# Kernel optimization log

Hardware: AMD Instinct MI355X
Metric: run time of the kernel (lower is better)

Reference implementation:

```python
import jax, jax.numpy as jnp
import numpy as np

B, L, D = 4, 2048, 512
H, DK = 8, 64          # n_heads, d_k = d_model // n_heads
DF = 2048              # d_ff
W = 9                  # window_size (odd so padding w//2 keeps L windows)


def setup_inputs() -> dict:
    key = jax.random.key(0)
    ks = jax.random.split(key, 12)
    s = 0.02
    p = lambda k, shp: (jax.random.normal(k, shp, jnp.float32) * s)
    return {
        "x": jax.random.normal(ks[0], (B, L, D), jnp.float32),
        "Wq": p(ks[1], (D, D)), "bq": jnp.zeros((D,), jnp.float32),
        "Wk": p(ks[2], (D, D)), "bk": jnp.zeros((D,), jnp.float32),
        "Wv": p(ks[3], (D, D)), "bv": jnp.zeros((D,), jnp.float32),
        "Wo": p(ks[4], (D, D)), "bo": jnp.zeros((D,), jnp.float32),
        "W1": p(ks[5], (D, DF)), "b1": jnp.zeros((DF,), jnp.float32),
        "W2": p(ks[6], (DF, D)), "b2": jnp.zeros((D,), jnp.float32),
        "g1": jnp.ones((D,), jnp.float32), "be1": jnp.zeros((D,), jnp.float32),
        "g2": jnp.ones((D,), jnp.float32), "be2": jnp.zeros((D,), jnp.float32),
    }


def _layer_norm(x, g, b, eps=1e-5):
    m = jnp.mean(x, axis=-1, keepdims=True)
    v = jnp.var(x, axis=-1, keepdims=True)
    return (x - m) * jax.lax.rsqrt(v + eps) * g + b


def reference(x, Wq, bq, Wk, bk, Wv, bv, Wo, bo, W1, b1, W2, b2, g1, be1, g2, be2):
    b, l, d = x.shape
    pad = W // 2
    padded = jnp.pad(x, ((0, 0), (pad, pad), (0, 0)))          # (B, L+W-1, D)
    idx = jnp.arange(l)[:, None] + jnp.arange(W)[None, :]       # (L, W)
    win = padded[:, idx]                                        # (B, L, W, D)

    # per-window full attention (Informer FullAttention, mask_flag=False)
    q = (win @ Wq + bq).reshape(b, l, W, H, DK)
    k = (win @ Wk + bk).reshape(b, l, W, H, DK)
    v = (win @ Wv + bv).reshape(b, l, W, H, DK)
    scale = 1.0 / jnp.sqrt(jnp.float32(DK))
    scores = jnp.einsum('blqhe,blkhe->blhqk', q, k) * scale     # (B, L, H, W, W)
    attn = jax.nn.softmax(scores, axis=-1)
    o = jnp.einsum('blhqk,blkhd->blqhd', attn, v).reshape(b, l, W, d)
    o = o @ Wo + bo                                             # (B, L, W, D)
    new_x = jnp.mean(o, axis=2)                                 # mean-pool over window

    x1 = _layer_norm(x + new_x, g1, be1)

    # pointwise conv FFN (kernel_size=1 Conv1d == Linear), exact GELU
    h = jax.nn.gelu(x1 @ W1 + b1, approximate=False)
    y = h @ W2 + b2
    return _layer_norm(x1 + y, g2, be2)
```

## Files before the change

kernel.cpp:

```cpp
#include <hip/hip_runtime.h>


typedef unsigned short u16;
typedef __attribute__((ext_vector_type(8))) short short8;
typedef __attribute__((ext_vector_type(4))) float floatx4;

#define DEV static __device__ __forceinline__

DEV float b2f(u16 u) {
  union { unsigned int i; float f; } x; x.i = ((unsigned int)u) << 16; return x.f;
}
DEV u16 f2b(float f) {
  union { float f; unsigned int i; } x; x.f = f;
  unsigned int u = x.i + 0x7fffu + ((x.i >> 16) & 1u);
  return (u16)(u >> 16);
}

#define AS1 __attribute__((address_space(1)))
#define AS3 __attribute__((address_space(3)))
DEV void gload_lds16(const void* g, void* l) {
  __builtin_amdgcn_global_load_lds((const AS1 void*)g, (AS3 void*)l, 16, 0, 0);
}

__global__ __launch_bounds__(256) void prep_all(
    const float* __restrict__ Wq, const float* __restrict__ Wk,
    const float* __restrict__ Wo, const float* __restrict__ W1,
    const float* __restrict__ W2, const float* __restrict__ Wv,
    const float* __restrict__ bq, const float* __restrict__ bk,
    const float* __restrict__ bv, const float* __restrict__ x,
    u16* __restrict__ WqkvT, u16* __restrict__ WoT,
    u16* __restrict__ W1T, u16* __restrict__ W2T, u16* __restrict__ Wvb,
    float* __restrict__ bqkv, u16* __restrict__ xb) {
  const int bid = blockIdx.x;
  if (bid >= 3080) {
    const int i = (bid - 3080) * 256 + threadIdx.x;
    float4 v = ((const float4*)x)[i];
    ushort4 o;
    o.x = f2b(v.x); o.y = f2b(v.y); o.z = f2b(v.z); o.w = f2b(v.w);
    ((ushort4*)xb)[i] = o;
    return;
  }
  if (bid >= 3072) {
    const int i = (bid - 3072) * 256 + threadIdx.x;
    if (i < 512) bqkv[i] = bq[i];
    else if (i < 1024) bqkv[i] = bk[i - 512];
    else if (i < 1536) {
      const int c = i - 1024;
      float s = 0.f;
      for (int j = 0; j < 512; ++j) s += bv[j] * Wo[(size_t)j * 512 + c];
      bqkv[i] = s;
    } else bqkv[i] = 0.f;
    return;
  }
  if (bid >= 2816) {
    const int i = (bid - 2816) * 256 + threadIdx.x;
    float4 v = ((const float4*)Wv)[i];
    ushort4 o;
    o.x = f2b(v.x); o.y = f2b(v.y); o.z = f2b(v.z); o.w = f2b(v.w);
    ((ushort4*)Wvb)[i] = o;
    return;
  }
  const float* in; u16* out; int R, C, t;
  if (bid < 256)       { in = Wq; out = WqkvT;          R = 512;  C = 512;  t = bid; }
  else if (bid < 512)  { in = Wk; out = WqkvT + 262144; R = 512;  C = 512;  t = bid - 256; }
  else if (bid < 768)  { in = Wo; out = WoT;            R = 512;  C = 512;  t = bid - 512; }
  else if (bid < 1792) { in = W1; out = W1T;            R = 512;  C = 2048; t = bid - 768; }
  else                 { in = W2; out = W2T;            R = 2048; C = 512;  t = bid - 1792; }
  const int tpr = C >> 5;
  const int bc = (t % tpr) * 32, br = (t / tpr) * 32;
  __shared__ float tile[32][33];
  const int tx = threadIdx.x & 31, ty = threadIdx.x >> 5;
  #pragma unroll
  for (int i = 0; i < 32; i += 8)
    tile[ty + i][tx] = in[(size_t)(br + ty + i) * C + bc + tx];
  __syncthreads();
  #pragma unroll
  for (int i = 0; i < 32; i += 8)
    out[(size_t)(bc + ty + i) * R + br + tx] = f2b(tile[tx][ty + i]);
}

template<int EPI>
__global__ __launch_bounds__(256, 4) void gemm_bt(
    const u16* __restrict__ A, const u16* __restrict__ BT,
    const float* __restrict__ bias, u16* __restrict__ C,
    int M, int N, int lda, int kb) {
  __shared__ __align__(16) u16 As[3][4096];
  __shared__ __align__(16) u16 Bs[3][2048];
  const int tid = threadIdx.x;
  const int w = tid >> 6, l = tid & 63;
  const int l15 = l & 15, l4 = l >> 4;
  const int wr = w & 1, wc = w >> 1;

  const int gx = (int)gridDim.x, gy = (int)gridDim.y;
  int id = (int)blockIdx.y * gx + (int)blockIdx.x;
  const int nwg = gx * gy;
  if ((nwg & 7) == 0) { const int cpx = nwg >> 3; id = (id & 7) * cpx + (id >> 3); }
  const int bx = id % gx; const int by = id / gx;
  const int bm = by * 128, bn = bx * 64;

  const int row0 = tid >> 2;
  const int kc0 = ((((tid & 3) - ((tid >> 3) & 3)) & 3)) * 8;
  const u16* gA = A  + (size_t)(bm + row0) * lda + kc0;
  const u16* gB = BT + (size_t)(bn + row0) * lda + kc0;
  const size_t a1 = (size_t)64 * lda;
  const int sd = w * 512 + l * 8;

  const int rg8 = ((l4 + ((l15 >> 1) & 3)) & 3) * 8;
  const int aBase = (wr * 64 + l15) * 32 + rg8;
  const int bBase = (wc * 32 + l15) * 32 + rg8;

  floatx4 acc[4][2] = {};
  const int nt = kb >> 5;

  auto stage = [&](int t, int buf) {
    const u16* a = gA + (size_t)t * 32;
    const u16* b = gB + (size_t)t * 32;
    gload_lds16(a,      &As[buf][sd]);
    gload_lds16(a + a1, &As[buf][2048 + sd]);
    gload_lds16(b,      &Bs[buf][sd]);
  };

  stage(0, 0);
  stage(1, 1);
  asm volatile("s_waitcnt vmcnt(3)" ::: "memory");
  __builtin_amdgcn_s_barrier();
  asm volatile("" ::: "memory");

  int cur = 0;
  for (int t = 0; t < nt; ++t) {
    int sb = cur + 2; if (sb >= 3) sb -= 3;
    const bool pf = (t + 2 < nt);
    if (pf) stage(t + 2, sb);

    short8 af[4], bf[2];
    #pragma unroll
    for (int m = 0; m < 4; ++m) af[m] = *(const short8*)(&As[cur][aBase + m * 512]);
    #pragma unroll
    for (int n = 0; n < 2; ++n) bf[n] = *(const short8*)(&Bs[cur][bBase + n * 512]);
    #pragma unroll
    for (int m = 0; m < 4; ++m)
      #pragma unroll
      for (int n = 0; n < 2; ++n)
        acc[m][n] = __builtin_amdgcn_mfma_f32_16x16x32_bf16(af[m], bf[n], acc[m][n], 0, 0, 0);

    if (pf) asm volatile("s_waitcnt vmcnt(3)" ::: "memory");
    else    asm volatile("s_waitcnt vmcnt(0)" ::: "memory");
    __builtin_amdgcn_s_barrier();
    asm volatile("" ::: "memory");

    cur = (cur == 2) ? 0 : cur + 1;
  }

  const int col0 = bn + wc * 32 + l15;
  float bvv[2];
  #pragma unroll
  for (int n = 0; n < 2; ++n) bvv[n] = bias[col0 + n * 16];
  #pragma unroll
  for (int m = 0; m < 4; ++m) {
    #pragma unroll
    for (int ri = 0; ri < 4; ++ri) {
      const size_t row = (size_t)(bm + wr * 64 + m * 16 + l4 * 4 + ri);
      u16* cp = C + row * N + col0;
      #pragma unroll
      for (int n = 0; n < 2; ++n) {
        float vv = acc[m][n][ri] + bvv[n];
        if (EPI == 1) {
          const float u = vv * (1.0f + 0.044715f * vv * vv);
          vv = vv / (1.0f + __expf(-1.5957691216057308f * u));
        }
        cp[n * 16] = f2b(vv);
      }
    }
  }
}

#define ATL 32
#define ART (ATL + 8)

__global__ __launch_bounds__(256) void attn_band(
    const u16* __restrict__ QKV, const float* __restrict__ bqkv,
    const float* __restrict__ bo, u16* __restrict__ newx) {
  __shared__ __align__(16) u16 S3[3][ART][72];
  __shared__ float Gb[ART][18];
  __shared__ float Sm[ART][81];
  __shared__ float Wb[ATL][9];

  const int tid = threadIdx.x;
  const int bid = ((int)blockIdx.x & 7) * 256 + ((int)blockIdx.x >> 3);
  const int h = bid & 7;
  const int chunk = (bid >> 3) & 63;
  const int b = bid >> 9;
  const int l0 = chunk * ATL;

  for (int idx = tid; idx < ART * 24; idx += 256) {
    const int ti = idx / 24, c = idx % 24;
    const int slice = c >> 3, d8 = (c & 7) * 8;
    const int col = slice * 512 + h * 64 + d8;
    const int t = l0 - 4 + ti;
    short8 v;
    if ((unsigned)t < 2048u) {
      v = *(const short8*)(QKV + ((size_t)((b << 11) | t)) * 1536 + col);
    } else {
      #pragma unroll
      for (int j = 0; j < 8; ++j) v[j] = (short)f2b(bqkv[col + j]);
    }
    *(short8*)(&S3[slice][ti][d8]) = v;
  }
  __syncthreads();

  for (int task = tid; task < ART * 17; task += 256) {
    const int ti = task / 17, j = task % 17;
    const int ui = ti + j - 8;
    if ((unsigned)ui < (unsigned)ART) {
      float a = 0.f;
      #pragma unroll
      for (int d0 = 0; d0 < 64; d0 += 8) {
        short8 qv = *(const short8*)(&S3[0][ti][d0]);
        short8 kv = *(const short8*)(&S3[1][ui][d0]);
        #pragma unroll
        for (int jj = 0; jj < 8; ++jj) a += b2f((u16)qv[jj]) * b2f((u16)kv[jj]);
      }
      Gb[ti][j] = a * 0.125f;
    }
  }
  __syncthreads();

  for (int task = tid; task < ART * 9; task += 256) {
    const int ti = task / 9, qw = task % 9;
    const int li = ti - qw;
    if ((unsigned)li < (unsigned)ATL) {
      float m = -1e30f;
      #pragma unroll
      for (int kw = 0; kw < 9; ++kw) m = fmaxf(m, Gb[ti][kw - qw + 8]);
      float e[9], s = 0.f;
      #pragma unroll
      for (int kw = 0; kw < 9; ++kw) { e[kw] = expf(Gb[ti][kw - qw + 8] - m); s += e[kw]; }
      const float inv = 1.f / s;
      #pragma unroll
      for (int kw = 0; kw < 9; ++kw) Sm[ti][qw * 9 + kw] = e[kw] * inv;
    }
  }
  __syncthreads();

  for (int task = tid; task < ATL * 9; task += 256) {
    const int li = task / 9, kw = task % 9;
    float s = 0.f;
    #pragma unroll
    for (int qw = 0; qw < 9; ++qw) s += Sm[li + qw][qw * 9 + kw];
    Wb[li][kw] = s * (1.f / 9.f);
  }
  __syncthreads();

  {
    const int li = tid >> 3, d8 = (tid & 7) * 8;
    float w[9];
    #pragma unroll
    for (int kw = 0; kw < 9; ++kw) w[kw] = Wb[li][kw];
    float a[8] = {};
    #pragma unroll
    for (int kw = 0; kw < 9; ++kw) {
      short8 vv = *(const short8*)(&S3[2][li + kw][d8]);
      #pragma unroll
      for (int jj = 0; jj < 8; ++jj) a[jj] += w[kw] * b2f((u16)vv[jj]);
    }
    short8 o;
    #pragma unroll
    for (int jj = 0; jj < 8; ++jj) o[jj] = (short)f2b(a[jj] + bo[h * 64 + d8 + jj]);
    const int l = l0 + li;
    *(short8*)(newx + ((size_t)((b << 11) | l)) * 512 + h * 64 + d8) = o;
  }
}

template<int MODE>
__global__ __launch_bounds__(256) void ln_kernel(
    const u16* __restrict__ a, const u16* __restrict__ bsrc,
    const float* __restrict__ g, const float* __restrict__ be,
    u16* __restrict__ outb, float* __restrict__ outf) {
  const int wave = threadIdx.x >> 6, lane = threadIdx.x & 63;
  const size_t row = (size_t)blockIdx.x * 4 + wave;
  const size_t base = row * 512 + lane * 8;
  const int gi = lane * 8;
  float v[8];
  short8 a8 = *(const short8*)(a + base);
  short8 b8 = *(const short8*)(bsrc + base);
  #pragma unroll
  for (int j = 0; j < 8; ++j) v[j] = b2f((u16)a8[j]) + b2f((u16)b8[j]);

  float s = 0.f;
  #pragma unroll
  for (int j = 0; j < 8; ++j) s += v[j];
  #pragma unroll
  for (int off = 32; off >= 1; off >>= 1) s += __shfl_xor(s, off, 64);
  const float mean = s * (1.f / 512.f);
  float sq = 0.f;
  #pragma unroll
  for (int j = 0; j < 8; ++j) { float d = v[j] - mean; sq += d * d; }
  #pragma unroll
  for (int off = 32; off >= 1; off >>= 1) sq += __shfl_xor(sq, off, 64);
  const float rs = rsqrtf(sq * (1.f / 512.f) + 1e-5f);

  if (MODE == 0) {
    short8 o;
    #pragma unroll
    for (int j = 0; j < 8; ++j)
      o[j] = (short)f2b((v[j] - mean) * rs * g[gi + j] + be[gi + j]);
    *(short8*)(outb + base) = o;
  } else {
    float4 o0, o1;
    o0.x = (v[0] - mean) * rs * g[gi + 0] + be[gi + 0];
    o0.y = (v[1] - mean) * rs * g[gi + 1] + be[gi + 1];
    o0.z = (v[2] - mean) * rs * g[gi + 2] + be[gi + 2];
    o0.w = (v[3] - mean) * rs * g[gi + 3] + be[gi + 3];
    o1.x = (v[4] - mean) * rs * g[gi + 4] + be[gi + 4];
    o1.y = (v[5] - mean) * rs * g[gi + 5] + be[gi + 5];
    o1.z = (v[6] - mean) * rs * g[gi + 6] + be[gi + 6];
    o1.w = (v[7] - mean) * rs * g[gi + 7] + be[gi + 7];
    *(float4*)(outf + base) = o0;
    *(float4*)(outf + base + 4) = o1;
  }
}

extern "C" void kernel_launch(void* const* d_in, const int* in_sizes, int n_in,
                              void* d_out, int out_size, void* d_ws, size_t ws_size,
                              hipStream_t stream) {
  const float* x   = (const float*)d_in[0];
  const float* Wq  = (const float*)d_in[1];
  const float* bq  = (const float*)d_in[2];
  const float* Wk  = (const float*)d_in[3];
  const float* bk  = (const float*)d_in[4];
  const float* Wv  = (const float*)d_in[5];
  const float* bv  = (const float*)d_in[6];
  const float* Wo  = (const float*)d_in[7];
  const float* bo  = (const float*)d_in[8];
  const float* W1  = (const float*)d_in[9];
  const float* b1  = (const float*)d_in[10];
  const float* W2  = (const float*)d_in[11];
  const float* b2  = (const float*)d_in[12];
  const float* g1  = (const float*)d_in[13];
  const float* be1 = (const float*)d_in[14];
  const float* g2  = (const float*)d_in[15];
  const float* be2 = (const float*)d_in[16];

  char* w = (char*)d_ws;
  u16*   xb    = (u16*)  (w + 0);
  u16*   WqkvT = (u16*)  (w + 8388608);
  u16*   WoT   = (u16*)  (w + 9961472);
  u16*   W1T   = (u16*)  (w + 10485760);
  u16*   W2T   = (u16*)  (w + 12582912);
  float* bqkv  = (float*)(w + 14680064);
  u16*   Wvb   = (u16*)  (w + 14688256);
  u16*   QKV   = (u16*)  (w + 15212544);
  u16*   hbuf  = QKV;
  u16*   newx  = (u16*)  (w + 48766976);
  u16*   x1b   = (u16*)  (w + 57155584);
  u16*   WvoT  = WqkvT + 524288;
  u16*   ybuf  = newx;

  prep_all<<<7176, 256, 0, stream>>>(Wq, Wk, Wo, W1, W2, Wv, bq, bk, bv, x,
                                     WqkvT, WoT, W1T, W2T, Wvb, bqkv, xb);
  gemm_bt<0><<<dim3(8, 4), 256, 0, stream>>>(WoT, Wvb, bqkv + 1536, WvoT,
                                             512, 512, 512, 512);
  gemm_bt<0><<<dim3(24, 64), 256, 0, stream>>>(xb, WqkvT, bqkv, QKV,
                                               8192, 1536, 512, 512);
  attn_band<<<2048, 256, 0, stream>>>(QKV, bqkv, bo, newx);
  ln_kernel<0><<<2048, 256, 0, stream>>>(xb, newx, g1, be1, x1b, nullptr);
  gemm_bt<1><<<dim3(32, 64), 256, 0, stream>>>(x1b, W1T, b1, hbuf,
                                               8192, 2048, 512, 512);
  gemm_bt<0><<<dim3(8, 64), 256, 0, stream>>>(hbuf, W2T, b2, ybuf,
                                              8192, 512, 2048, 2048);
  ln_kernel<1><<<2048, 256, 0, stream>>>(x1b, ybuf, g2, be2, nullptr, (float*)d_out);
}
```

Measured before the change: 165.7 us.

## Give each wave private LDS staging to drop block barriers in GEMM

The GEMM now has each wave load its own A and B sub-tiles into a private LDS region through a 3-deep ring. This lets the main loop run with only per-wave vmcnt waits and no workgroup barriers. Waves no longer share operands, so every wave refetches the B rows that neighbouring waves also load, and A is duplicated across wave columns. Shared memory per block doubles to 72 KB and occupancy drops to 2 blocks per CU, trading more load traffic for less synchronisation stall.

```diff
diff --git a/kernel.cpp b/kernel.cpp
--- a/kernel.cpp
+++ b/kernel.cpp
@@ -80,12 +80,11 @@
 }
 
 template<int EPI>
-__global__ __launch_bounds__(256, 4) void gemm_bt(
+__global__ __launch_bounds__(256, 2) void gemm_wp(
     const u16* __restrict__ A, const u16* __restrict__ BT,
     const float* __restrict__ bias, u16* __restrict__ C,
     int M, int N, int lda, int kb) {
-  __shared__ __align__(16) u16 As[3][4096];
-  __shared__ __align__(16) u16 Bs[3][2048];
+  __shared__ __align__(16) u16 L[3][4][3072];
   const int tid = threadIdx.x;
   const int w = tid >> 6, l = tid & 63;
   const int l15 = l & 15, l4 = l >> 4;
@@ -98,56 +97,62 @@
   const int bx = id % gx; const int by = id / gx;
   const int bm = by * 128, bn = bx * 64;
 
-  const int row0 = tid >> 2;
-  const int kc0 = ((((tid & 3) - ((tid >> 3) & 3)) & 3)) * 8;
-  const u16* gA = A  + (size_t)(bm + row0) * lda + kc0;
-  const u16* gB = BT + (size_t)(bn + row0) * lda + kc0;
-  const size_t a1 = (size_t)64 * lda;
-  const int sd = w * 512 + l * 8;
+  const int srow = l >> 2;
+  const int kc0 = (((l & 3) - ((l >> 3) & 3)) & 3) * 8;
+  const u16* gA = A  + (size_t)(bm + wr * 64 + srow) * lda + kc0;
+  const u16* gB = BT + (size_t)(bn + wc * 32 + srow) * lda + kc0;
+  const size_t r16 = (size_t)16 * lda;
+  u16* const Lw0 = &L[0][w][0];
+  u16* const Lw1 = &L[1][w][0];
+  u16* const Lw2 = &L[2][w][0];
 
   const int rg8 = ((l4 + ((l15 >> 1) & 3)) & 3) * 8;
-  const int aBase = (wr * 64 + l15) * 32 + rg8;
-  const int bBase = (wc * 32 + l15) * 32 + rg8;
+  int aOff[4], bOff[2];
+  #pragma unroll
+  for (int m = 0; m < 4; ++m) aOff[m] = (m * 16 + l15) * 32 + rg8;
+  #pragma unroll
+  for (int n = 0; n < 2; ++n) bOff[n] = 2048 + (n * 16 + l15) * 32 + rg8;
 
   floatx4 acc[4][2] = {};
   const int nt = kb >> 5;
 
-  auto stage = [&](int t, int buf) {
+  auto stage = [&](int t, u16* d) {
     const u16* a = gA + (size_t)t * 32;
     const u16* b = gB + (size_t)t * 32;
-    gload_lds16(a,      &As[buf][sd]);
-    gload_lds16(a + a1, &As[buf][2048 + sd]);
-    gload_lds16(b,      &Bs[buf][sd]);
+    gload_lds16(a,            d);
+    gload_lds16(a + r16,      d + 512);
+    gload_lds16(a + 2 * r16,  d + 1024);
+    gload_lds16(a + 3 * r16,  d + 1536);
+    gload_lds16(b,            d + 2048);
+    gload_lds16(b + r16,      d + 2560);
   };
 
-  stage(0, 0);
-  stage(1, 1);
-  asm volatile("s_waitcnt vmcnt(3)" ::: "memory");
-  __builtin_amdgcn_s_barrier();
-  asm volatile("" ::: "memory");
+  stage(0, Lw0);
+  stage(1, Lw1);
 
   int cur = 0;
   for (int t = 0; t < nt; ++t) {
+    u16* const bufs[3] = {Lw0, Lw1, Lw2};
     int sb = cur + 2; if (sb >= 3) sb -= 3;
-    const bool pf = (t + 2 < nt);
-    if (pf) stage(t + 2, sb);
-
+    if (t + 2 < nt) {
+      stage(t + 2, bufs[sb]);
+      asm volatile("s_waitcnt vmcnt(12)" ::: "memory");
+    } else if (t + 1 < nt) {
+      asm volatile("s_waitcnt vmcnt(6)" ::: "memory");
+    } else {
+      asm volatile("s_waitcnt vmcnt(0)" ::: "memory");
+    }
+    const u16* Lb = bufs[cur];
     short8 af[4], bf[2];
     #pragma unroll
-    for (int m = 0; m < 4; ++m) af[m] = *(const short8*)(&As[cur][aBase + m * 512]);
-    #pragma unroll
-    for (int n = 0; n < 2; ++n) bf[n] = *(const short8*)(&Bs[cur][bBase + n * 512]);
+    for (int m = 0; m < 4; ++m) af[m] = *(const short8*)(Lb + aOff[m]);
+    #pragma unroll
+    for (int n = 0; n < 2; ++n) bf[n] = *(const short8*)(Lb + bOff[n]);
     #pragma unroll
     for (int m = 0; m < 4; ++m)
       #pragma unroll
       for (int n = 0; n < 2; ++n)
         acc[m][n] = __builtin_amdgcn_mfma_f32_16x16x32_bf16(af[m], bf[n], acc[m][n], 0, 0, 0);
-
-    if (pf) asm volatile("s_waitcnt vmcnt(3)" ::: "memory");
-    else    asm volatile("s_waitcnt vmcnt(0)" ::: "memory");
-    __builtin_amdgcn_s_barrier();
-    asm volatile("" ::: "memory");
-
     cur = (cur == 2) ? 0 : cur + 1;
   }
 
@@ -358,15 +363,15 @@
 
   prep_all<<<7176, 256, 0, stream>>>(Wq, Wk, Wo, W1, W2, Wv, bq, bk, bv, x,
                                      WqkvT, WoT, W1T, W2T, Wvb, bqkv, xb);
-  gemm_bt<0><<<dim3(8, 4), 256, 0, stream>>>(WoT, Wvb, bqkv + 1536, WvoT,
+  gemm_wp<0><<<dim3(8, 4), 256, 0, stream>>>(WoT, Wvb, bqkv + 1536, WvoT,
                                              512, 512, 512, 512);
-  gemm_bt<0><<<dim3(24, 64), 256, 0, stream>>>(xb, WqkvT, bqkv, QKV,
+  gemm_wp<0><<<dim3(24, 64), 256, 0, stream>>>(xb, WqkvT, bqkv, QKV,
                                                8192, 1536, 512, 512);
   attn_band<<<2048, 256, 0, stream>>>(QKV, bqkv, bo, newx);
   ln_kernel<0><<<2048, 256, 0, stream>>>(xb, newx, g1, be1, x1b, nullptr);
-  gemm_bt<1><<<dim3(32, 64), 256, 0, stream>>>(x1b, W1T, b1, hbuf,
+  gemm_wp<1><<<dim3(32, 64), 256, 0, stream>>>(x1b, W1T, b1, hbuf,
                                                8192, 2048, 512, 512);
-  gemm_bt<0><<<dim3(8, 64), 256, 0, stream>>>(hbuf, W2T, b2, ybuf,
+  gemm_wp<0><<<dim3(8, 64), 256, 0, stream>>>(hbuf, W2T, b2, ybuf,
                                               8192, 512, 2048, 2048);
   ln_kernel<1><<<2048, 256, 0, stream>>>(x1b, ybuf, g2, be2, nullptr, (float*)d_out);
 }
```

New measurement: 217.3 us. 1.31x slower.

## Switch GEMM to double-buffered K=64 tiles with 8-way swizzled LDS layout

Applied to the files above, without the earlier changes.

The bf16 GEMM now stages 64-wide K slices into two LDS buffers instead of 32-wide slices into three, with an 8-chunk XOR-style swizzle and precomputed fragment offsets for the two K halves. Each iteration issues twice the MFMAs per barrier, which halves the barrier and wait count per unit of K. The cost is a shallower prefetch depth with a full vmcnt(0) wait each step, and larger LDS use, so occupancy is lowered to 3 blocks per CU in launch bounds.

```diff
diff --git a/kernel.cpp b/kernel.cpp
--- a/kernel.cpp
+++ b/kernel.cpp
@@ -80,12 +80,12 @@
 }
 
 template<int EPI>
-__global__ __launch_bounds__(256, 4) void gemm_bt(
+__global__ __launch_bounds__(256, 3) void gemm_bt(
     const u16* __restrict__ A, const u16* __restrict__ BT,
     const float* __restrict__ bias, u16* __restrict__ C,
     int M, int N, int lda, int kb) {
-  __shared__ __align__(16) u16 As[3][4096];
-  __shared__ __align__(16) u16 Bs[3][2048];
+  __shared__ __align__(16) u16 As[2][8192];
+  __shared__ __align__(16) u16 Bs[2][4096];
   const int tid = threadIdx.x;
   const int w = tid >> 6, l = tid & 63;
   const int l15 = l & 15, l4 = l >> 4;
@@ -98,57 +98,68 @@
   const int bx = id % gx; const int by = id / gx;
   const int bm = by * 128, bn = bx * 64;
 
-  const int row0 = tid >> 2;
-  const int kc0 = ((((tid & 3) - ((tid >> 3) & 3)) & 3)) * 8;
-  const u16* gA = A  + (size_t)(bm + row0) * lda + kc0;
-  const u16* gB = BT + (size_t)(bn + row0) * lda + kc0;
-  const size_t a1 = (size_t)64 * lda;
-  const int sd = w * 512 + l * 8;
-
-  const int rg8 = ((l4 + ((l15 >> 1) & 3)) & 3) * 8;
-  const int aBase = (wr * 64 + l15) * 32 + rg8;
-  const int bBase = (wc * 32 + l15) * 32 + rg8;
+  const int srow = tid >> 3;
+  const int sg8 = (((tid & 7) - (srow & 7)) & 7) * 8;
+  const u16* gA = A  + (size_t)(bm + srow) * lda + sg8;
+  const u16* gB = BT + (size_t)(bn + srow) * lda + sg8;
+  const size_t r32 = (size_t)32 * lda;
+  const int sd = tid * 8;
+
+  int aOff[2][4], bOff[2][2];
+  #pragma unroll
+  for (int kh = 0; kh < 2; ++kh) {
+    #pragma unroll
+    for (int m = 0; m < 4; ++m) {
+      const int r = wr * 64 + m * 16 + l15;
+      aOff[kh][m] = r * 64 + (((l4 + 4 * kh) + (r & 7)) & 7) * 8;
+    }
+    #pragma unroll
+    for (int n = 0; n < 2; ++n) {
+      const int r = wc * 32 + n * 16 + l15;
+      bOff[kh][n] = r * 64 + (((l4 + 4 * kh) + (r & 7)) & 7) * 8;
+    }
+  }
 
   floatx4 acc[4][2] = {};
-  const int nt = kb >> 5;
+  const int nt = kb >> 6;
 
   auto stage = [&](int t, int buf) {
-    const u16* a = gA + (size_t)t * 32;
-    const u16* b = gB + (size_t)t * 32;
-    gload_lds16(a,      &As[buf][sd]);
-    gload_lds16(a + a1, &As[buf][2048 + sd]);
-    gload_lds16(b,      &Bs[buf][sd]);
+    const u16* a = gA + (size_t)t * 64;
+    const u16* b = gB + (size_t)t * 64;
+    gload_lds16(a,           &As[buf][sd]);
+    gload_lds16(a + r32,     &As[buf][2048 + sd]);
+    gload_lds16(a + 2 * r32, &As[buf][4096 + sd]);
+    gload_lds16(a + 3 * r32, &As[buf][6144 + sd]);
+    gload_lds16(b,           &Bs[buf][sd]);
+    gload_lds16(b + r32,     &Bs[buf][2048 + sd]);
   };
 
   stage(0, 0);
-  stage(1, 1);
-  asm volatile("s_waitcnt vmcnt(3)" ::: "memory");
+  asm volatile("s_waitcnt vmcnt(0)" ::: "memory");
   __builtin_amdgcn_s_barrier();
   asm volatile("" ::: "memory");
 
-  int cur = 0;
   for (int t = 0; t < nt; ++t) {
-    int sb = cur + 2; if (sb >= 3) sb -= 3;
-    const bool pf = (t + 2 < nt);
-    if (pf) stage(t + 2, sb);
-
-    short8 af[4], bf[2];
-    #pragma unroll
-    for (int m = 0; m < 4; ++m) af[m] = *(const short8*)(&As[cur][aBase + m * 512]);
-    #pragma unroll
-    for (int n = 0; n < 2; ++n) bf[n] = *(const short8*)(&Bs[cur][bBase + n * 512]);
-    #pragma unroll
-    for (int m = 0; m < 4; ++m)
-      #pragma unroll
-      for (int n = 0; n < 2; ++n)
-        acc[m][n] = __builtin_amdgcn_mfma_f32_16x16x32_bf16(af[m], bf[n], acc[m][n], 0, 0, 0);
-
-    if (pf) asm volatile("s_waitcnt vmcnt(3)" ::: "memory");
-    else    asm volatile("s_waitcnt vmcnt(0)" ::: "memory");
+    const int cur = t & 1;
+    if (t + 1 < nt) stage(t + 1, cur ^ 1);
+
+    #pragma unroll
+    for (int kh = 0; kh < 2; ++kh) {
+      short8 af[4], bf[2];
+      #pragma unroll
+      for (int m = 0; m < 4; ++m) af[m] = *(const short8*)(&As[cur][aOff[kh][m]]);
+      #pragma unroll
+      for (int n = 0; n < 2; ++n) bf[n] = *(const short8*)(&Bs[cur][bOff[kh][n]]);
+      #pragma unroll
+      for (int m = 0; m < 4; ++m)
+        #pragma unroll
+        for (int n = 0; n < 2; ++n)
+          acc[m][n] = __builtin_amdgcn_mfma_f32_16x16x32_bf16(af[m], bf[n], acc[m][n], 0, 0, 0);
+    }
+
+    asm volatile("s_waitcnt vmcnt(0)" ::: "memory");
     __builtin_amdgcn_s_barrier();
     asm volatile("" ::: "memory");
-
-    cur = (cur == 2) ? 0 : cur + 1;
   }
 
   const int col0 = bn + wc * 32 + l15;
```

Result: faster. 145.0 us, median of 2 (-12.5%).
